# Optimization experiments

Measured on AMD Instinct MI355X. Metric: run time of the kernel, lower is better.

## Reference

```python
import jax, jax.numpy as jnp
import numpy as np

NUM_USERS = 400000  # matches fill_max of indexes in input_specs
K = 10              # top_k from init_kwargs
NEG_INF = -1000000000.0


def setup_inputs() -> dict:
    key = jax.random.key(0)
    k1, k2, k3 = jax.random.split(key, 3)
    N = 8000000
    predictions = jax.random.normal(k1, (N,), dtype=jnp.float32)
    targets = jax.random.uniform(k2, (N,), dtype=jnp.float32)
    indexes = jax.random.randint(k3, (N,), 0, NUM_USERS, dtype=jnp.int64)
    return {"predictions": predictions, "targets": targets, "indexes": indexes}


def reference(predictions, targets, indexes):
    # Faithful to the torch source, which does `counts_per_user[u] = 1` (not +=1):
    # column 0 holds each user's FIRST occurrence, column 1 holds the LAST
    # occurrence (subsequent scatters to pos 1 overwrite), everything else is
    # padding (-1e9 preds / 0 targets). Padding columns beyond k provably don't
    # affect topk/dcg/idcg, so we use a static width of K.
    n = predictions.shape[0]
    pos = jnp.arange(n, dtype=jnp.int32)
    seg = indexes.astype(jnp.int32)
    first = jax.ops.segment_min(pos, seg, num_segments=NUM_USERS)
    last = jax.ops.segment_max(pos, seg, num_segments=NUM_USERS)
    counts = jax.ops.segment_sum(jnp.ones_like(pos), seg, num_segments=NUM_USERS)
    has2 = counts >= 2  # pos 1 is only ever written on a second occurrence

    p0 = predictions[first]
    t0 = targets[first]
    p1 = jnp.where(has2, predictions[last], NEG_INF)
    t1 = jnp.where(has2, targets[last], 0.0)

    pred_padded = jnp.full((NUM_USERS, K), NEG_INF, dtype=predictions.dtype)
    pred_padded = pred_padded.at[:, 0].set(p0).at[:, 1].set(p1)
    target_padded = jnp.zeros((NUM_USERS, K), dtype=targets.dtype)
    target_padded = target_padded.at[:, 0].set(t0).at[:, 1].set(t1)

    _, topk_idx = jax.lax.top_k(pred_padded, K)
    topk_targets = jnp.take_along_axis(target_padded, topk_idx, axis=1)
    discounts = jnp.log2(jnp.arange(2, K + 2, dtype=jnp.float32))
    dcg = (topk_targets / discounts).sum(axis=1)
    ideal = -jnp.sort(-target_padded, axis=1)  # descending sort
    idcg = (ideal[:, :K] / discounts).sum(axis=1)
    return (dcg / idcg).mean()
```

## Files before the change

### kernel.cpp

```cpp
#include <hip/hip_runtime.h>
#include <climits>

static constexpr int NUSERS = 400000;
static constexpr float NEG_INF_F = -1000000000.0f;
static constexpr float INV_LOG2_3 = 0.6309297535714575f;

static constexpr int USLICE = 1563;
static constexpr int S = 256;
static constexpr int CHUNK = 4096;
static constexpr int CPG = 255;
static constexpr int GSPAN = CHUNK * CPG;
static constexpr int G = 8;
static constexpr int CAP = 4608;


__global__ void k_init_part(int* __restrict__ cursor, float* __restrict__ acc) {
    int t = blockIdx.x * blockDim.x + threadIdx.x;
    if (t < G * S) cursor[t] = 0;
    if (t == G * S) acc[0] = 0.0f;
}

__global__ __launch_bounds__(256, 8) void k_scatter(const int* __restrict__ idx, int n,
                                                    unsigned* __restrict__ records,
                                                    int* __restrict__ cursor) {
    __shared__ int cnt[S];
    __shared__ int base_l[S + 1];
    __shared__ int base_g[S];
    __shared__ unsigned stage[CHUNK];

    const int t = threadIdx.x;
    const int g = blockIdx.x / CPG;
    const int cbase = blockIdx.x * CHUNK - g * GSPAN;
    const int q0 = blockIdx.x * (CHUNK / 4);
    const int nq = n >> 2;
    const int4* idx4 = reinterpret_cast<const int4*>(idx);

    int4 v[4];
    int rnk[16];
#pragma unroll
    for (int k = 0; k < 4; ++k) {
        int q = q0 + k * 256 + t;
        v[k] = (q < nq) ? idx4[q] : make_int4(-1, -1, -1, -1);
    }

    if (t < S) cnt[t] = 0;
    __syncthreads();

#pragma unroll
    for (int k = 0; k < 4; ++k) {
        int us[4] = {v[k].x, v[k].y, v[k].z, v[k].w};
#pragma unroll
        for (int e = 0; e < 4; ++e)
            rnk[k * 4 + e] = (us[e] >= 0) ? atomicAdd(&cnt[us[e] / USLICE], 1) : 0;
    }
    __syncthreads();

    if (t < 64) {
        int v0 = cnt[t];
        int v1 = cnt[64 + t];
        int v2 = cnt[128 + t];
        int v3 = cnt[192 + t];
        int a = v0, b = v1, c = v2, d = v3;
#pragma unroll
        for (int dd = 1; dd < 64; dd <<= 1) { int y = __shfl_up(a, dd, 64); if (t >= dd) a += y; }
        int ta = __shfl(a, 63, 64);
#pragma unroll
        for (int dd = 1; dd < 64; dd <<= 1) { int y = __shfl_up(b, dd, 64); if (t >= dd) b += y; }
        int tb = __shfl(b, 63, 64);
#pragma unroll
        for (int dd = 1; dd < 64; dd <<= 1) { int y = __shfl_up(c, dd, 64); if (t >= dd) c += y; }
        int tc = __shfl(c, 63, 64);
#pragma unroll
        for (int dd = 1; dd < 64; dd <<= 1) { int y = __shfl_up(d, dd, 64); if (t >= dd) d += y; }
        int td = __shfl(d, 63, 64);
        b += ta; c += ta + tb; d += ta + tb + tc;
        base_l[t] = a - v0;
        base_l[64 + t] = b - v1;
        base_l[128 + t] = c - v2;
        base_l[192 + t] = d - v3;
        if (t == 0) base_l[S] = ta + tb + tc + td;
    }
    if (t < S) base_g[t] = atomicAdd(&cursor[g * S + t], cnt[t]);
    __syncthreads();

#pragma unroll
    for (int k = 0; k < 4; ++k) {
        int us[4] = {v[k].x, v[k].y, v[k].z, v[k].w};
#pragma unroll
        for (int e = 0; e < 4; ++e) {
            int u = us[e];
            if (u >= 0) {
                int s = u / USLICE;
                int loc = u - s * USLICE;
                int pos = base_l[s] + rnk[k * 4 + e];
                unsigned pic = (unsigned)((k * 256 + t) * 4 + e);
                stage[pos] = ((unsigned)s << 23) | ((unsigned)loc << 12) | pic;
            }
        }
    }
    __syncthreads();

    int total = base_l[S];
    for (int r = t; r < total; r += 256) {
        unsigned tmp = stage[r];
        int s = tmp >> 23;
        unsigned loc = (tmp >> 12) & 0x7FFu;
        unsigned iloc = (unsigned)cbase + (tmp & 0xFFFu);
        int pos = base_g[s] + (r - base_l[s]);
        if (pos < CAP)
            records[(size_t)(g * S + s) * CAP + pos] = (loc << 20) | iloc;
    }
}

__global__ __launch_bounds__(1024, 4) void k_reduce_ndcg(
        const unsigned* __restrict__ records, const int* __restrict__ cursor,
        const float* __restrict__ pred, const float* __restrict__ tgt,
        int n, float* __restrict__ acc) {
    __shared__ int tabf[USLICE];
    __shared__ int tabl[USLICE];
    const int s = blockIdx.x;
    const int t = threadIdx.x;

    for (int u = t; u < USLICE; u += 1024) { tabf[u] = INT_MAX; tabl[u] = -1; }
    __syncthreads();

    for (int g = 0; g < G; ++g) {
        int cnt = min(cursor[g * S + s], CAP);
        const uint4* base4 = reinterpret_cast<const uint4*>(records + (size_t)(g * S + s) * CAP);
        const int gb = g * GSPAN;
        for (int p4 = t; p4 * 4 < cnt; p4 += 1024) {
            uint4 vv = base4[p4];
            int p = p4 * 4;
            unsigned rr[4] = {vv.x, vv.y, vv.z, vv.w};
#pragma unroll
            for (int e = 0; e < 4; ++e) {
                if (p + e < cnt) {
                    int loc = rr[e] >> 20;
                    int i = (int)(rr[e] & 0xFFFFFu) + gb;
                    atomicMin(&tabf[loc], i);
                    atomicMax(&tabl[loc], i);
                }
            }
        }
    }
    __syncthreads();

    float v = 0.0f;
    for (int uu = t; uu < USLICE; uu += 1024) {
        int u = s * USLICE + uu;
        if (u < NUSERS) {
            int f = tabf[uu];
            int l = tabl[uu];
            f = min(f, n - 1);
            float p0 = pred[f];
            float t0 = tgt[f];
            bool has2 = l > f;
            float p1 = has2 ? pred[l] : NEG_INF_F;
            float t1 = has2 ? tgt[l] : 0.0f;
            float dcg  = (p0 >= p1) ? fmaf(t1, INV_LOG2_3, t0) : fmaf(t0, INV_LOG2_3, t1);
            float idcg = fmaf(fminf(t0, t1), INV_LOG2_3, fmaxf(t0, t1));
            v += dcg / idcg;
        }
    }
    for (int off = 32; off > 0; off >>= 1) v += __shfl_down(v, off, 64);
    __shared__ float wsum[16];
    int lane = t & 63, wid = t >> 6;
    if (lane == 0) wsum[wid] = v;
    __syncthreads();
    if (t == 0) {
        float ss = 0.0f;
#pragma unroll
        for (int w = 0; w < 16; ++w) ss += wsum[w];
        atomicAdd(acc, ss);
    }
}

__global__ void k_final(const float* __restrict__ acc, float* __restrict__ out) {
    out[0] = acc[0] * (1.0f / (float)NUSERS);
}


__global__ void k_init_fb(int* __restrict__ first, int* __restrict__ last,
                          float* __restrict__ acc) {
    int i = blockIdx.x * blockDim.x + threadIdx.x;
    if (i < NUSERS) { first[i] = INT_MAX; last[i] = -1; }
    if (i == 0) acc[0] = 0.0f;
}

__global__ void k_minmax_fb(const int* __restrict__ idx, int* __restrict__ first,
                            int* __restrict__ last, int n) {
    int base = (blockIdx.x * blockDim.x + threadIdx.x) * 4;
    if (base + 3 < n) {
        int4 u4 = *reinterpret_cast<const int4*>(idx + base);
        int us[4] = {u4.x, u4.y, u4.z, u4.w};
#pragma unroll
        for (int j = 0; j < 4; ++j) {
            int u = us[j], i = base + j;
            if (i < first[u]) atomicMin(&first[u], i);
            if (i > last[u])  atomicMax(&last[u], i);
        }
    } else {
        for (int i = base; i < n; ++i) {
            int u = idx[i];
            if (i < first[u]) atomicMin(&first[u], i);
            if (i > last[u])  atomicMax(&last[u], i);
        }
    }
}

__global__ void k_ndcg_fb(const float* __restrict__ pred, const float* __restrict__ tgt,
                          const int* __restrict__ first, const int* __restrict__ last,
                          int n, float* __restrict__ acc) {
    int u = blockIdx.x * blockDim.x + threadIdx.x;
    float v = 0.0f;
    if (u < NUSERS) {
        int f = min(first[u], n - 1);
        int l = last[u];
        float p0 = pred[f], t0 = tgt[f];
        bool has2 = l > f;
        float p1 = has2 ? pred[l] : NEG_INF_F;
        float t1 = has2 ? tgt[l] : 0.0f;
        float dcg  = (p0 >= p1) ? fmaf(t1, INV_LOG2_3, t0) : fmaf(t0, INV_LOG2_3, t1);
        float idcg = fmaf(fminf(t0, t1), INV_LOG2_3, fmaxf(t0, t1));
        v = dcg / idcg;
    }
    for (int off = 32; off > 0; off >>= 1) v += __shfl_down(v, off, 64);
    __shared__ float wsum[4];
    int lane = threadIdx.x & 63, wid = threadIdx.x >> 6;
    if (lane == 0) wsum[wid] = v;
    __syncthreads();
    if (threadIdx.x == 0) atomicAdd(acc, wsum[0] + wsum[1] + wsum[2] + wsum[3]);
}


extern "C" void kernel_launch(void* const* d_in, const int* in_sizes, int n_in,
                              void* d_out, int out_size, void* d_ws, size_t ws_size,
                              hipStream_t stream) {
    const float* pred = (const float*)d_in[0];
    const float* tgt  = (const float*)d_in[1];
    const int*   idx  = (const int*)d_in[2];
    const int n = in_sizes[0];
    float* out = (float*)d_out;

    const size_t recs_bytes = (size_t)G * S * CAP * sizeof(unsigned);
    const size_t need = recs_bytes + 16384;

    if (ws_size >= need && n <= G * GSPAN && (n & 3) == 0) {
        unsigned* records = (unsigned*)d_ws;
        char* tail = (char*)d_ws + recs_bytes;
        int* cursor = (int*)tail;
        float* acc = (float*)(tail + 8192);

        k_init_part<<<(G * S + 256) / 256, 256, 0, stream>>>(cursor, acc);

        int nblocks = (n + CHUNK - 1) / CHUNK;
        k_scatter<<<nblocks, 256, 0, stream>>>(idx, n, records, cursor);

        k_reduce_ndcg<<<S, 1024, 0, stream>>>(records, cursor, pred, tgt, n, acc);

        k_final<<<1, 1, 0, stream>>>(acc, out);
    } else {
        int* first = (int*)d_ws;
        int* last  = first + NUSERS;
        float* acc = (float*)(last + NUSERS);

        k_init_fb<<<(NUSERS + 255) / 256, 256, 0, stream>>>(first, last, acc);
        int nq4 = (n + 3) / 4;
        k_minmax_fb<<<(nq4 + 255) / 256, 256, 0, stream>>>(idx, first, last, n);
        k_ndcg_fb<<<(NUSERS + 255) / 256, 256, 0, stream>>>(pred, tgt, first, last, n, acc);
        k_final<<<1, 1, 0, stream>>>(acc, out);
    }
}
```

Baseline: 151.1 us.

## Fuse scatter and reduce into one persistent kernel with grid barrier

```diff
diff --git a/kernel.cpp b/kernel.cpp
--- a/kernel.cpp
+++ b/kernel.cpp
@@ -7,138 +7,160 @@
 
 static constexpr int USLICE = 1563;
 static constexpr int S = 256;
-static constexpr int CHUNK = 4096;
-static constexpr int CPG = 255;
+static constexpr int CHUNK = 8192;
+static constexpr int CPG = 256;
 static constexpr int GSPAN = CHUNK * CPG;
-static constexpr int G = 8;
-static constexpr int CAP = 4608;
-
-
-__global__ void k_init_part(int* __restrict__ cursor, float* __restrict__ acc) {
-    int t = blockIdx.x * blockDim.x + threadIdx.x;
-    if (t < G * S) cursor[t] = 0;
-    if (t == G * S) acc[0] = 0.0f;
-}
-
-__global__ __launch_bounds__(256, 8) void k_scatter(const int* __restrict__ idx, int n,
-                                                    unsigned* __restrict__ records,
-                                                    int* __restrict__ cursor) {
-    __shared__ int cnt[S];
-    __shared__ int base_l[S + 1];
-    __shared__ int base_g[S];
-    __shared__ unsigned stage[CHUNK];
+static constexpr int G = 4;
+static constexpr int CAP = 9216;
+static constexpr int NB = 256;
+static constexpr int NT = 1024;
+
+struct ScatterSh {
+    int cnt[S];
+    int base_l[S + 1];
+    int base_g[S];
+    unsigned stage[CHUNK];
+};
+struct ReduceSh {
+    int2 tab[USLICE];
+    float wsum[16];
+};
+
+__global__ void k_init(int* __restrict__ cursor, int* __restrict__ ctrl,
+                       float* __restrict__ acc) {
+    int t = threadIdx.x;
+    cursor[t] = 0;
+    if (t < 16) ctrl[t] = 0;
+    if (t == 16) acc[0] = 0.0f;
+}
+
+__global__ __launch_bounds__(NT, 4) void k_fused(
+        const int* __restrict__ idx, int n,
+        unsigned* __restrict__ records, int* __restrict__ cursor,
+        int* __restrict__ ctrl,
+        const float* __restrict__ pred, const float* __restrict__ tgt,
+        float* __restrict__ acc, float* __restrict__ out, int nchunks) {
+    __shared__ union { ScatterSh sc; ReduceSh rd; } sh;
+    __shared__ int curchunk;
 
     const int t = threadIdx.x;
-    const int g = blockIdx.x / CPG;
-    const int cbase = blockIdx.x * CHUNK - g * GSPAN;
-    const int q0 = blockIdx.x * (CHUNK / 4);
     const int nq = n >> 2;
     const int4* idx4 = reinterpret_cast<const int4*>(idx);
 
-    int4 v[4];
-    int rnk[16];
-#pragma unroll
-    for (int k = 0; k < 4; ++k) {
-        int q = q0 + k * 256 + t;
-        v[k] = (q < nq) ? idx4[q] : make_int4(-1, -1, -1, -1);
-    }
-
-    if (t < S) cnt[t] = 0;
-    __syncthreads();
-
-#pragma unroll
-    for (int k = 0; k < 4; ++k) {
-        int us[4] = {v[k].x, v[k].y, v[k].z, v[k].w};
-#pragma unroll
-        for (int e = 0; e < 4; ++e)
-            rnk[k * 4 + e] = (us[e] >= 0) ? atomicAdd(&cnt[us[e] / USLICE], 1) : 0;
-    }
-    __syncthreads();
-
-    if (t < 64) {
-        int v0 = cnt[t];
-        int v1 = cnt[64 + t];
-        int v2 = cnt[128 + t];
-        int v3 = cnt[192 + t];
-        int a = v0, b = v1, c = v2, d = v3;
-#pragma unroll
-        for (int dd = 1; dd < 64; dd <<= 1) { int y = __shfl_up(a, dd, 64); if (t >= dd) a += y; }
-        int ta = __shfl(a, 63, 64);
-#pragma unroll
-        for (int dd = 1; dd < 64; dd <<= 1) { int y = __shfl_up(b, dd, 64); if (t >= dd) b += y; }
-        int tb = __shfl(b, 63, 64);
-#pragma unroll
-        for (int dd = 1; dd < 64; dd <<= 1) { int y = __shfl_up(c, dd, 64); if (t >= dd) c += y; }
-        int tc = __shfl(c, 63, 64);
-#pragma unroll
-        for (int dd = 1; dd < 64; dd <<= 1) { int y = __shfl_up(d, dd, 64); if (t >= dd) d += y; }
-        int td = __shfl(d, 63, 64);
-        b += ta; c += ta + tb; d += ta + tb + tc;
-        base_l[t] = a - v0;
-        base_l[64 + t] = b - v1;
-        base_l[128 + t] = c - v2;
-        base_l[192 + t] = d - v3;
-        if (t == 0) base_l[S] = ta + tb + tc + td;
-    }
-    if (t < S) base_g[t] = atomicAdd(&cursor[g * S + t], cnt[t]);
-    __syncthreads();
-
-#pragma unroll
-    for (int k = 0; k < 4; ++k) {
-        int us[4] = {v[k].x, v[k].y, v[k].z, v[k].w};
-#pragma unroll
-        for (int e = 0; e < 4; ++e) {
+    for (;;) {
+        if (t == 0) curchunk = atomicAdd(&ctrl[0], 1);
+        __syncthreads();
+        const int c = curchunk;
+        if (c >= nchunks) break;
+        const int g = c >> 8;
+        const int cbase = c * CHUNK - g * GSPAN;
+        const int q0 = c * (CHUNK / 4);
+
+        int4 v0, v1;
+        { int q = q0 + t;      v0 = (q < nq) ? idx4[q] : make_int4(-1, -1, -1, -1); }
+        { int q = q0 + NT + t; v1 = (q < nq) ? idx4[q] : make_int4(-1, -1, -1, -1); }
+
+        if (t < S) sh.sc.cnt[t] = 0;
+        __syncthreads();
+
+        unsigned tmp[8];
+        int rnk[8];
+        int us[8] = {v0.x, v0.y, v0.z, v0.w, v1.x, v1.y, v1.z, v1.w};
+#pragma unroll
+        for (int e = 0; e < 8; ++e) {
             int u = us[e];
             if (u >= 0) {
-                int s = u / USLICE;
-                int loc = u - s * USLICE;
-                int pos = base_l[s] + rnk[k * 4 + e];
-                unsigned pic = (unsigned)((k * 256 + t) * 4 + e);
-                stage[pos] = ((unsigned)s << 23) | ((unsigned)loc << 12) | pic;
+                int sb = u / USLICE;
+                int loc = u - sb * USLICE;
+                unsigned pic = (e < 4) ? (unsigned)(t * 4 + e)
+                                       : (unsigned)((NT + t) * 4 + (e - 4));
+                rnk[e] = atomicAdd(&sh.sc.cnt[sb], 1);
+                tmp[e] = ((unsigned)sb << 24) | ((unsigned)loc << 13) | pic;
+            } else {
+                rnk[e] = -1;
+                tmp[e] = 0;
             }
         }
-    }
-    __syncthreads();
-
-    int total = base_l[S];
-    for (int r = t; r < total; r += 256) {
-        unsigned tmp = stage[r];
-        int s = tmp >> 23;
-        unsigned loc = (tmp >> 12) & 0x7FFu;
-        unsigned iloc = (unsigned)cbase + (tmp & 0xFFFu);
-        int pos = base_g[s] + (r - base_l[s]);
-        if (pos < CAP)
-            records[(size_t)(g * S + s) * CAP + pos] = (loc << 20) | iloc;
-    }
-}
-
-__global__ __launch_bounds__(1024, 4) void k_reduce_ndcg(
-        const unsigned* __restrict__ records, const int* __restrict__ cursor,
-        const float* __restrict__ pred, const float* __restrict__ tgt,
-        int n, float* __restrict__ acc) {
-    __shared__ int tabf[USLICE];
-    __shared__ int tabl[USLICE];
+        __syncthreads();
+
+        if (t < 64) {
+            int c0 = sh.sc.cnt[t];
+            int c1 = sh.sc.cnt[64 + t];
+            int c2 = sh.sc.cnt[128 + t];
+            int c3 = sh.sc.cnt[192 + t];
+            int a = c0, b = c1, cc = c2, d = c3;
+#pragma unroll
+            for (int dd = 1; dd < 64; dd <<= 1) { int y = __shfl_up(a, dd, 64); if (t >= dd) a += y; }
+            int ta = __shfl(a, 63, 64);
+#pragma unroll
+            for (int dd = 1; dd < 64; dd <<= 1) { int y = __shfl_up(b, dd, 64); if (t >= dd) b += y; }
+            int tb = __shfl(b, 63, 64);
+#pragma unroll
+            for (int dd = 1; dd < 64; dd <<= 1) { int y = __shfl_up(cc, dd, 64); if (t >= dd) cc += y; }
+            int tc = __shfl(cc, 63, 64);
+#pragma unroll
+            for (int dd = 1; dd < 64; dd <<= 1) { int y = __shfl_up(d, dd, 64); if (t >= dd) d += y; }
+            int td = __shfl(d, 63, 64);
+            b += ta; cc += ta + tb; d += ta + tb + tc;
+            sh.sc.base_l[t] = a - c0;
+            sh.sc.base_l[64 + t] = b - c1;
+            sh.sc.base_l[128 + t] = cc - c2;
+            sh.sc.base_l[192 + t] = d - c3;
+            if (t == 0) sh.sc.base_l[S] = ta + tb + tc + td;
+        }
+        if (t < S) sh.sc.base_g[t] = atomicAdd(&cursor[g * S + t], sh.sc.cnt[t]);
+        __syncthreads();
+
+#pragma unroll
+        for (int e = 0; e < 8; ++e) {
+            if (rnk[e] >= 0) {
+                int sb = (int)(tmp[e] >> 24);
+                sh.sc.stage[sh.sc.base_l[sb] + rnk[e]] = tmp[e];
+            }
+        }
+        __syncthreads();
+
+        const int total = sh.sc.base_l[S];
+        for (int r = t; r < total; r += NT) {
+            unsigned w = sh.sc.stage[r];
+            int sb = (int)(w >> 24);
+            unsigned loc = (w >> 13) & 0x7FFu;
+            unsigned iloc = (unsigned)cbase + (w & 0x1FFFu);
+            int pos = sh.sc.base_g[sb] + (r - sh.sc.base_l[sb]);
+            if (pos < CAP)
+                records[(size_t)(g * S + sb) * CAP + pos] = (loc << 21) | iloc;
+        }
+    }
+
+    __threadfence();
+    __syncthreads();
+    if (t == 0) {
+        __hip_atomic_fetch_add(&ctrl[1], 1, __ATOMIC_ACQ_REL, __HIP_MEMORY_SCOPE_AGENT);
+        while (__hip_atomic_load(&ctrl[1], __ATOMIC_ACQUIRE, __HIP_MEMORY_SCOPE_AGENT) < NB)
+            __builtin_amdgcn_s_sleep(2);
+    }
+    __syncthreads();
+
     const int s = blockIdx.x;
-    const int t = threadIdx.x;
-
-    for (int u = t; u < USLICE; u += 1024) { tabf[u] = INT_MAX; tabl[u] = -1; }
+    for (int uu = t; uu < USLICE; uu += NT) sh.rd.tab[uu] = make_int2(INT_MAX, -1);
     __syncthreads();
 
     for (int g = 0; g < G; ++g) {
         int cnt = min(cursor[g * S + s], CAP);
         const uint4* base4 = reinterpret_cast<const uint4*>(records + (size_t)(g * S + s) * CAP);
         const int gb = g * GSPAN;
-        for (int p4 = t; p4 * 4 < cnt; p4 += 1024) {
+        for (int p4 = t; p4 * 4 < cnt; p4 += NT) {
             uint4 vv = base4[p4];
             int p = p4 * 4;
             unsigned rr[4] = {vv.x, vv.y, vv.z, vv.w};
 #pragma unroll
             for (int e = 0; e < 4; ++e) {
                 if (p + e < cnt) {
-                    int loc = rr[e] >> 20;
-                    int i = (int)(rr[e] & 0xFFFFFu) + gb;
-                    atomicMin(&tabf[loc], i);
-                    atomicMax(&tabl[loc], i);
+                    int loc = (int)(rr[e] >> 21);
+                    int i = (int)(rr[e] & 0x1FFFFFu) + gb;
+                    int2 cur = sh.rd.tab[loc];
+                    if (cur.x > i) atomicMin(&sh.rd.tab[loc].x, i);
+                    if (cur.y < i) atomicMax(&sh.rd.tab[loc].y, i);
                 }
             }
         }
@@ -146,12 +168,12 @@
     __syncthreads();
 
     float v = 0.0f;
-    for (int uu = t; uu < USLICE; uu += 1024) {
+    for (int uu = t; uu < USLICE; uu += NT) {
         int u = s * USLICE + uu;
         if (u < NUSERS) {
-            int f = tabf[uu];
-            int l = tabl[uu];
-            f = min(f, n - 1);
+            int2 fl = sh.rd.tab[uu];
+            int f = min(fl.x, n - 1);
+            int l = fl.y;
             float p0 = pred[f];
             float t0 = tgt[f];
             bool has2 = l > f;
@@ -163,20 +185,20 @@
         }
     }
     for (int off = 32; off > 0; off >>= 1) v += __shfl_down(v, off, 64);
-    __shared__ float wsum[16];
     int lane = t & 63, wid = t >> 6;
-    if (lane == 0) wsum[wid] = v;
+    if (lane == 0) sh.rd.wsum[wid] = v;
     __syncthreads();
     if (t == 0) {
         float ss = 0.0f;
 #pragma unroll
-        for (int w = 0; w < 16; ++w) ss += wsum[w];
+        for (int w = 0; w < 16; ++w) ss += sh.rd.wsum[w];
         atomicAdd(acc, ss);
-    }
-}
-
-__global__ void k_final(const float* __restrict__ acc, float* __restrict__ out) {
-    out[0] = acc[0] * (1.0f / (float)NUSERS);
+        int d = __hip_atomic_fetch_add(&ctrl[2], 1, __ATOMIC_ACQ_REL, __HIP_MEMORY_SCOPE_AGENT);
+        if (d == NB - 1) {
+            float a = __hip_atomic_load(acc, __ATOMIC_RELAXED, __HIP_MEMORY_SCOPE_AGENT);
+            out[0] = a * (1.0f / (float)NUSERS);
+        }
+    }
 }
 
 
@@ -232,6 +254,10 @@
     if (threadIdx.x == 0) atomicAdd(acc, wsum[0] + wsum[1] + wsum[2] + wsum[3]);
 }
 
+__global__ void k_final_fb(const float* __restrict__ acc, float* __restrict__ out) {
+    out[0] = acc[0] * (1.0f / (float)NUSERS);
+}
+
 
 extern "C" void kernel_launch(void* const* d_in, const int* in_sizes, int n_in,
                               void* d_out, int out_size, void* d_ws, size_t ws_size,
@@ -243,22 +269,19 @@
     float* out = (float*)d_out;
 
     const size_t recs_bytes = (size_t)G * S * CAP * sizeof(unsigned);
-    const size_t need = recs_bytes + 16384;
-
-    if (ws_size >= need && n <= G * GSPAN && (n & 3) == 0) {
+    const size_t need = recs_bytes + 4096 + 256;
+
+    if (ws_size >= need && n <= G * GSPAN && (n & 3) == 0 && n >= 4) {
         unsigned* records = (unsigned*)d_ws;
-        char* tail = (char*)d_ws + recs_bytes;
-        int* cursor = (int*)tail;
-        float* acc = (float*)(tail + 8192);
-
-        k_init_part<<<(G * S + 256) / 256, 256, 0, stream>>>(cursor, acc);
-
-        int nblocks = (n + CHUNK - 1) / CHUNK;
-        k_scatter<<<nblocks, 256, 0, stream>>>(idx, n, records, cursor);
-
-        k_reduce_ndcg<<<S, 1024, 0, stream>>>(records, cursor, pred, tgt, n, acc);
-
-        k_final<<<1, 1, 0, stream>>>(acc, out);
+        int* cursor = (int*)((char*)d_ws + recs_bytes);
+        int* ctrl = cursor + G * S;
+        float* acc = (float*)(ctrl + 16);
+
+        k_init<<<1, NT, 0, stream>>>(cursor, ctrl, acc);
+
+        int nchunks = (n + CHUNK - 1) / CHUNK;
+        k_fused<<<NB, NT, 0, stream>>>(idx, n, records, cursor, ctrl,
+                                       pred, tgt, acc, out, nchunks);
     } else {
         int* first = (int*)d_ws;
         int* last  = first + NUSERS;
@@ -268,6 +291,6 @@
         int nq4 = (n + 3) / 4;
         k_minmax_fb<<<(nq4 + 255) / 256, 256, 0, stream>>>(idx, first, last, n);
         k_ndcg_fb<<<(NUSERS + 255) / 256, 256, 0, stream>>>(pred, tgt, first, last, n, acc);
-        k_final<<<1, 1, 0, stream>>>(acc, out);
-    }
-}
+        k_final_fb<<<1, 1, 0, stream>>>(acc, out);
+    }
+}
```

After: 268.0 us. 77.3% more time.

## Split reduce into half-slice blocks, fewer chunk groups, fuse final step

Applied to the files above, without the earlier changes.

```diff
diff --git a/kernel.cpp b/kernel.cpp
--- a/kernel.cpp
+++ b/kernel.cpp
@@ -6,18 +6,21 @@
 static constexpr float INV_LOG2_3 = 0.6309297535714575f;
 
 static constexpr int USLICE = 1563;
+static constexpr int HALF = 782;
 static constexpr int S = 256;
 static constexpr int CHUNK = 4096;
-static constexpr int CPG = 255;
+static constexpr int CPG = 512;
 static constexpr int GSPAN = CHUNK * CPG;
-static constexpr int G = 8;
-static constexpr int CAP = 4608;
-
-
-__global__ void k_init_part(int* __restrict__ cursor, float* __restrict__ acc) {
-    int t = blockIdx.x * blockDim.x + threadIdx.x;
-    if (t < G * S) cursor[t] = 0;
-    if (t == G * S) acc[0] = 0.0f;
+static constexpr int G = 4;
+static constexpr int CAP = 8960;
+
+
+__global__ void k_init_part(int* __restrict__ cursor, int* __restrict__ ctrl,
+                            float* __restrict__ acc) {
+    int t = threadIdx.x;
+    cursor[t] = 0;
+    if (t < 16) ctrl[t] = 0;
+    if (t == 16) acc[0] = 0.0f;
 }
 
 __global__ __launch_bounds__(256, 8) void k_scatter(const int* __restrict__ idx, int n,
@@ -29,7 +32,7 @@
     __shared__ unsigned stage[CHUNK];
 
     const int t = threadIdx.x;
-    const int g = blockIdx.x / CPG;
+    const int g = blockIdx.x >> 9;
     const int cbase = blockIdx.x * CHUNK - g * GSPAN;
     const int q0 = blockIdx.x * (CHUNK / 4);
     const int nq = n >> 2;
@@ -108,20 +111,25 @@
         unsigned iloc = (unsigned)cbase + (tmp & 0xFFFu);
         int pos = base_g[s] + (r - base_l[s]);
         if (pos < CAP)
-            records[(size_t)(g * S + s) * CAP + pos] = (loc << 20) | iloc;
-    }
-}
-
-__global__ __launch_bounds__(1024, 4) void k_reduce_ndcg(
+            records[(size_t)(g * S + s) * CAP + pos] = (loc << 21) | iloc;
+    }
+}
+
+__global__ __launch_bounds__(1024, 8) void k_reduce_ndcg(
         const unsigned* __restrict__ records, const int* __restrict__ cursor,
         const float* __restrict__ pred, const float* __restrict__ tgt,
-        int n, float* __restrict__ acc) {
-    __shared__ int tabf[USLICE];
-    __shared__ int tabl[USLICE];
-    const int s = blockIdx.x;
+        int n, float* __restrict__ acc, int* __restrict__ ctrl,
+        float* __restrict__ out, int nblk) {
+    __shared__ int tabf[HALF];
+    __shared__ int tabl[HALF];
+    __shared__ float wsum[16];
+    const int s = blockIdx.x >> 1;
+    const int half = blockIdx.x & 1;
+    const int lo = half * HALF;
+    const int nloc = min(USLICE - lo, HALF);
     const int t = threadIdx.x;
 
-    for (int u = t; u < USLICE; u += 1024) { tabf[u] = INT_MAX; tabl[u] = -1; }
+    for (int u = t; u < nloc; u += 1024) { tabf[u] = INT_MAX; tabl[u] = -1; }
     __syncthreads();
 
     for (int g = 0; g < G; ++g) {
@@ -135,10 +143,12 @@
 #pragma unroll
             for (int e = 0; e < 4; ++e) {
                 if (p + e < cnt) {
-                    int loc = rr[e] >> 20;
-                    int i = (int)(rr[e] & 0xFFFFFu) + gb;
-                    atomicMin(&tabf[loc], i);
-                    atomicMax(&tabl[loc], i);
+                    unsigned lr = (rr[e] >> 21) - (unsigned)lo;
+                    if (lr < (unsigned)nloc) {
+                        int i = (int)(rr[e] & 0x1FFFFFu) + gb;
+                        atomicMin(&tabf[lr], i);
+                        atomicMax(&tabl[lr], i);
+                    }
                 }
             }
         }
@@ -146,24 +156,25 @@
     __syncthreads();
 
     float v = 0.0f;
-    for (int uu = t; uu < USLICE; uu += 1024) {
-        int u = s * USLICE + uu;
+    for (int uu = t; uu < nloc; uu += 1024) {
+        int u = s * USLICE + lo + uu;
         if (u < NUSERS) {
-            int f = tabf[uu];
+            int f = min(tabf[uu], n - 1);
             int l = tabl[uu];
-            f = min(f, n - 1);
+            int lc = max(l, 0);
             float p0 = pred[f];
             float t0 = tgt[f];
+            float p1v = pred[lc];
+            float t1v = tgt[lc];
             bool has2 = l > f;
-            float p1 = has2 ? pred[l] : NEG_INF_F;
-            float t1 = has2 ? tgt[l] : 0.0f;
+            float p1 = has2 ? p1v : NEG_INF_F;
+            float t1 = has2 ? t1v : 0.0f;
             float dcg  = (p0 >= p1) ? fmaf(t1, INV_LOG2_3, t0) : fmaf(t0, INV_LOG2_3, t1);
             float idcg = fmaf(fminf(t0, t1), INV_LOG2_3, fmaxf(t0, t1));
             v += dcg / idcg;
         }
     }
     for (int off = 32; off > 0; off >>= 1) v += __shfl_down(v, off, 64);
-    __shared__ float wsum[16];
     int lane = t & 63, wid = t >> 6;
     if (lane == 0) wsum[wid] = v;
     __syncthreads();
@@ -172,11 +183,12 @@
 #pragma unroll
         for (int w = 0; w < 16; ++w) ss += wsum[w];
         atomicAdd(acc, ss);
-    }
-}
-
-__global__ void k_final(const float* __restrict__ acc, float* __restrict__ out) {
-    out[0] = acc[0] * (1.0f / (float)NUSERS);
+        int d = __hip_atomic_fetch_add(&ctrl[2], 1, __ATOMIC_ACQ_REL, __HIP_MEMORY_SCOPE_AGENT);
+        if (d == nblk - 1) {
+            float a = __hip_atomic_load(acc, __ATOMIC_RELAXED, __HIP_MEMORY_SCOPE_AGENT);
+            out[0] = a * (1.0f / (float)NUSERS);
+        }
+    }
 }
 
 
@@ -232,6 +244,10 @@
     if (threadIdx.x == 0) atomicAdd(acc, wsum[0] + wsum[1] + wsum[2] + wsum[3]);
 }
 
+__global__ void k_final_fb(const float* __restrict__ acc, float* __restrict__ out) {
+    out[0] = acc[0] * (1.0f / (float)NUSERS);
+}
+
 
 extern "C" void kernel_launch(void* const* d_in, const int* in_sizes, int n_in,
                               void* d_out, int out_size, void* d_ws, size_t ws_size,
@@ -243,22 +259,22 @@
     float* out = (float*)d_out;
 
     const size_t recs_bytes = (size_t)G * S * CAP * sizeof(unsigned);
-    const size_t need = recs_bytes + 16384;
-
-    if (ws_size >= need && n <= G * GSPAN && (n & 3) == 0) {
+    const size_t need = recs_bytes + 8192;
+
+    if (ws_size >= need && n <= G * GSPAN && (n & 3) == 0 && n >= 4) {
         unsigned* records = (unsigned*)d_ws;
         char* tail = (char*)d_ws + recs_bytes;
         int* cursor = (int*)tail;
-        float* acc = (float*)(tail + 8192);
-
-        k_init_part<<<(G * S + 256) / 256, 256, 0, stream>>>(cursor, acc);
+        int* ctrl = cursor + G * S;
+        float* acc = (float*)(ctrl + 16);
+
+        k_init_part<<<1, 1024, 0, stream>>>(cursor, ctrl, acc);
 
         int nblocks = (n + CHUNK - 1) / CHUNK;
         k_scatter<<<nblocks, 256, 0, stream>>>(idx, n, records, cursor);
 
-        k_reduce_ndcg<<<S, 1024, 0, stream>>>(records, cursor, pred, tgt, n, acc);
-
-        k_final<<<1, 1, 0, stream>>>(acc, out);
+        k_reduce_ndcg<<<2 * S, 1024, 0, stream>>>(records, cursor, pred, tgt, n,
+                                                  acc, ctrl, out, 2 * S);
     } else {
         int* first = (int*)d_ws;
         int* last  = first + NUSERS;
@@ -268,6 +284,6 @@
         int nq4 = (n + 3) / 4;
         k_minmax_fb<<<(nq4 + 255) / 256, 256, 0, stream>>>(idx, first, last, n);
         k_ndcg_fb<<<(NUSERS + 255) / 256, 256, 0, stream>>>(pred, tgt, first, last, n, acc);
-        k_final<<<1, 1, 0, stream>>>(acc, out);
-    }
-}
+        k_final_fb<<<1, 1, 0, stream>>>(acc, out);
+    }
+}
```

Result: slower. 173.2 us (+14.6%).

## Prefetch pred/tgt into cache during scatter, fuse final kernel, check LDS atomics first

Applied to the files above, without the earlier changes.

```diff
diff --git a/kernel.cpp b/kernel.cpp
--- a/kernel.cpp
+++ b/kernel.cpp
@@ -14,15 +14,11 @@
 static constexpr int CAP = 4608;
 
 
-__global__ void k_init_part(int* __restrict__ cursor, float* __restrict__ acc) {
-    int t = blockIdx.x * blockDim.x + threadIdx.x;
-    if (t < G * S) cursor[t] = 0;
-    if (t == G * S) acc[0] = 0.0f;
-}
-
 __global__ __launch_bounds__(256, 8) void k_scatter(const int* __restrict__ idx, int n,
                                                     unsigned* __restrict__ records,
-                                                    int* __restrict__ cursor) {
+                                                    int* __restrict__ cursor,
+                                                    const float* __restrict__ pred,
+                                                    const float* __restrict__ tgt) {
     __shared__ int cnt[S];
     __shared__ int base_l[S + 1];
     __shared__ int base_g[S];
@@ -34,13 +30,21 @@
     const int q0 = blockIdx.x * (CHUNK / 4);
     const int nq = n >> 2;
     const int4* idx4 = reinterpret_cast<const int4*>(idx);
+    const float4* pred4 = reinterpret_cast<const float4*>(pred);
+    const float4* tgt4 = reinterpret_cast<const float4*>(tgt);
 
     int4 v[4];
     int rnk[16];
+    float warm = 0.0f;
 #pragma unroll
     for (int k = 0; k < 4; ++k) {
         int q = q0 + k * 256 + t;
         v[k] = (q < nq) ? idx4[q] : make_int4(-1, -1, -1, -1);
+        if (q < nq) {
+            float4 a = pred4[q];
+            float4 b = tgt4[q];
+            warm += a.x + a.y + a.z + a.w + b.x + b.y + b.z + b.w;
+        }
     }
 
     if (t < S) cnt[t] = 0;
@@ -110,14 +114,17 @@
         if (pos < CAP)
             records[(size_t)(g * S + s) * CAP + pos] = (loc << 20) | iloc;
     }
+    asm volatile("" :: "v"(warm));
 }
 
 __global__ __launch_bounds__(1024, 4) void k_reduce_ndcg(
         const unsigned* __restrict__ records, const int* __restrict__ cursor,
         const float* __restrict__ pred, const float* __restrict__ tgt,
-        int n, float* __restrict__ acc) {
+        int n, float* __restrict__ acc, int* __restrict__ ctrl,
+        float* __restrict__ out) {
     __shared__ int tabf[USLICE];
     __shared__ int tabl[USLICE];
+    __shared__ float wsum[16];
     const int s = blockIdx.x;
     const int t = threadIdx.x;
 
@@ -137,8 +144,8 @@
                 if (p + e < cnt) {
                     int loc = rr[e] >> 20;
                     int i = (int)(rr[e] & 0xFFFFFu) + gb;
-                    atomicMin(&tabf[loc], i);
-                    atomicMax(&tabl[loc], i);
+                    if (i < tabf[loc]) atomicMin(&tabf[loc], i);
+                    if (i > tabl[loc]) atomicMax(&tabl[loc], i);
                 }
             }
         }
@@ -146,24 +153,34 @@
     __syncthreads();
 
     float v = 0.0f;
-    for (int uu = t; uu < USLICE; uu += 1024) {
-        int u = s * USLICE + uu;
-        if (u < NUSERS) {
-            int f = tabf[uu];
-            int l = tabl[uu];
-            f = min(f, n - 1);
-            float p0 = pred[f];
-            float t0 = tgt[f];
-            bool has2 = l > f;
-            float p1 = has2 ? pred[l] : NEG_INF_F;
-            float t1 = has2 ? tgt[l] : 0.0f;
-            float dcg  = (p0 >= p1) ? fmaf(t1, INV_LOG2_3, t0) : fmaf(t0, INV_LOG2_3, t1);
-            float idcg = fmaf(fminf(t0, t1), INV_LOG2_3, fmaxf(t0, t1));
+    {
+        const int u0 = s * USLICE + t;
+        const int u1 = u0 + 1024;
+        const bool a0 = (u0 < NUSERS);
+        const bool a1 = (t + 1024 < USLICE) && (u1 < NUSERS);
+        int f0 = a0 ? min(tabf[t], n - 1) : 0;
+        int l0 = a0 ? tabl[t] : -1;
+        int f1 = a1 ? min(tabf[t + 1024], n - 1) : 0;
+        int l1 = a1 ? tabl[t + 1024] : -1;
+        int c0 = max(l0, 0), c1 = max(l1, 0);
+        float p00 = pred[f0], q00 = tgt[f0], p01 = pred[c0], q01 = tgt[c0];
+        float p10 = pred[f1], q10 = tgt[f1], p11 = pred[c1], q11 = tgt[c1];
+        if (a0) {
+            bool h = l0 > f0;
+            float pb = h ? p01 : NEG_INF_F, qb = h ? q01 : 0.0f;
+            float dcg  = (p00 >= pb) ? fmaf(qb, INV_LOG2_3, q00) : fmaf(q00, INV_LOG2_3, qb);
+            float idcg = fmaf(fminf(q00, qb), INV_LOG2_3, fmaxf(q00, qb));
             v += dcg / idcg;
         }
+        if (a1) {
+            bool h = l1 > f1;
+            float pb = h ? p11 : NEG_INF_F, qb = h ? q11 : 0.0f;
+            float dcg  = (p10 >= pb) ? fmaf(qb, INV_LOG2_3, q10) : fmaf(q10, INV_LOG2_3, qb);
+            float idcg = fmaf(fminf(q10, qb), INV_LOG2_3, fmaxf(q10, qb));
+            v += dcg / idcg;
+        }
     }
     for (int off = 32; off > 0; off >>= 1) v += __shfl_down(v, off, 64);
-    __shared__ float wsum[16];
     int lane = t & 63, wid = t >> 6;
     if (lane == 0) wsum[wid] = v;
     __syncthreads();
@@ -172,11 +189,12 @@
 #pragma unroll
         for (int w = 0; w < 16; ++w) ss += wsum[w];
         atomicAdd(acc, ss);
-    }
-}
-
-__global__ void k_final(const float* __restrict__ acc, float* __restrict__ out) {
-    out[0] = acc[0] * (1.0f / (float)NUSERS);
+        int d = __hip_atomic_fetch_add(&ctrl[0], 1, __ATOMIC_ACQ_REL, __HIP_MEMORY_SCOPE_AGENT);
+        if (d == S - 1) {
+            float a = __hip_atomic_load(acc, __ATOMIC_RELAXED, __HIP_MEMORY_SCOPE_AGENT);
+            out[0] = a * (1.0f / (float)NUSERS);
+        }
+    }
 }
 
 
@@ -232,6 +250,10 @@
     if (threadIdx.x == 0) atomicAdd(acc, wsum[0] + wsum[1] + wsum[2] + wsum[3]);
 }
 
+__global__ void k_final_fb(const float* __restrict__ acc, float* __restrict__ out) {
+    out[0] = acc[0] * (1.0f / (float)NUSERS);
+}
+
 
 extern "C" void kernel_launch(void* const* d_in, const int* in_sizes, int n_in,
                               void* d_out, int out_size, void* d_ws, size_t ws_size,
@@ -245,20 +267,20 @@
     const size_t recs_bytes = (size_t)G * S * CAP * sizeof(unsigned);
     const size_t need = recs_bytes + 16384;
 
-    if (ws_size >= need && n <= G * GSPAN && (n & 3) == 0) {
+    if (ws_size >= need && n <= G * GSPAN && (n & 3) == 0 && n >= 4) {
         unsigned* records = (unsigned*)d_ws;
         char* tail = (char*)d_ws + recs_bytes;
         int* cursor = (int*)tail;
-        float* acc = (float*)(tail + 8192);
-
-        k_init_part<<<(G * S + 256) / 256, 256, 0, stream>>>(cursor, acc);
+        int* ctrl = cursor + G * S;
+        float* acc = (float*)(ctrl + 16);
+
+        hipMemsetAsync(tail, 0, (size_t)(G * S + 16) * sizeof(int) + sizeof(float), stream);
 
         int nblocks = (n + CHUNK - 1) / CHUNK;
-        k_scatter<<<nblocks, 256, 0, stream>>>(idx, n, records, cursor);
-
-        k_reduce_ndcg<<<S, 1024, 0, stream>>>(records, cursor, pred, tgt, n, acc);
-
-        k_final<<<1, 1, 0, stream>>>(acc, out);
+        k_scatter<<<nblocks, 256, 0, stream>>>(idx, n, records, cursor, pred, tgt);
+
+        k_reduce_ndcg<<<S, 1024, 0, stream>>>(records, cursor, pred, tgt, n,
+                                              acc, ctrl, out);
     } else {
         int* first = (int*)d_ws;
         int* last  = first + NUSERS;
@@ -268,6 +290,6 @@
         int nq4 = (n + 3) / 4;
         k_minmax_fb<<<(nq4 + 255) / 256, 256, 0, stream>>>(idx, first, last, n);
         k_ndcg_fb<<<(NUSERS + 255) / 256, 256, 0, stream>>>(pred, tgt, first, last, n, acc);
-        k_final<<<1, 1, 0, stream>>>(acc, out);
-    }
-}
+        k_final_fb<<<1, 1, 0, stream>>>(acc, out);
+    }
+}
```

Result: slower. 174.3 us (+15.4%).
